# Kernel tuning notes

Measured on AMD Instinct MI355X. Metric: run time of the kernel, lower is better.

Reference implementation:

```python
import jax, jax.numpy as jnp
import numpy as np
import math

DIM, NH, HD = 4096, 32, 128
B, S = 2, 2048
MAX_SEQ, INIT_SLICE = 4096, 2048  # init_slice = max_seq_len - max_prompt_size
NEG = -1e9


def setup_inputs() -> dict:
    key = jax.random.key(0)
    ks = jax.random.split(key, 6)
    x = jax.random.normal(ks[0], (B, S, DIM), dtype=jnp.float32)
    scale = 1.0 / math.sqrt(DIM)
    wq = jax.random.normal(ks[1], (DIM, DIM), dtype=jnp.float32) * scale
    wk = jax.random.normal(ks[2], (DIM, DIM), dtype=jnp.float32) * scale
    wv = jax.random.normal(ks[3], (DIM, DIM), dtype=jnp.float32) * scale
    wo = jax.random.normal(ks[4], (DIM, DIM), dtype=jnp.float32) * scale
    # RoPE frequencies, viewed as real pairs [S, HD//2, 2] = (cos, sin)
    inv_freq = 1.0 / (10000.0 ** (jnp.arange(0, HD, 2, dtype=jnp.float32) / HD))
    ang = jnp.arange(S, dtype=jnp.float32)[:, None] * inv_freq[None, :]  # [S, HD//2]
    freqs_cis_real = jnp.stack([jnp.cos(ang), jnp.sin(ang)], axis=-1)
    # causal additive mask [1,1,S,S]
    mask = jnp.where(jnp.triu(jnp.ones((S, S), dtype=bool), k=1), NEG, 0.0)[None, None].astype(jnp.float32)
    cache_k = jnp.zeros((B, MAX_SEQ, NH, HD), dtype=jnp.float32)
    cache_v = jnp.zeros((B, MAX_SEQ, NH, HD), dtype=jnp.float32)
    return {"x": x, "freqs_cis_real": freqs_cis_real, "mask": mask,
            "wq": wq, "wk": wk, "wv": wv, "wo": wo,
            "cache_k": cache_k, "cache_v": cache_v, "slice_size": 2048}


def _apply_rotary(xq, xk, freqs_cis_real):
    # xq, xk: [b, s, h, d]; pairs along last dim are (real, imag)
    b, s, h, d = xq.shape
    fr = freqs_cis_real[None, :, None, :, 0]  # [1, s, 1, d//2]
    fi = freqs_cis_real[None, :, None, :, 1]

    def rot(t):
        t = t.reshape(b, s, h, d // 2, 2)
        tr, ti = t[..., 0], t[..., 1]
        out = jnp.stack([tr * fr - ti * fi, tr * fi + ti * fr], axis=-1)
        return out.reshape(b, s, h, d)

    return rot(xq), rot(xk)


def reference(x, freqs_cis_real, mask, wq, wk, wv, wo, cache_k, cache_v, slice_size):
    bsz, seqlen, _ = x.shape
    xq = (x @ wq.T).reshape(bsz, seqlen, NH, HD)
    xk = (x @ wk.T).reshape(bsz, seqlen, NH, HD)
    xv = (x @ wv.T).reshape(bsz, seqlen, NH, HD)
    xq, xk = _apply_rotary(xq, xk, freqs_cis_real)
    # prompt-phase (seqlen > 1) cache update: cat(cache[:, :init_slice], new)
    cache_k_new = jnp.concatenate([cache_k[:bsz, :INIT_SLICE], xk], axis=1)
    cache_v_new = jnp.concatenate([cache_v[:bsz, :INIT_SLICE], xv], axis=1)
    keys = cache_k_new[:, -slice_size:]    # [b, k, h, d]
    values = cache_v_new[:, -slice_size:]
    scores = jnp.einsum('bqhd,bkhd->bhqk', xq, keys) / math.sqrt(HD)
    scores = scores + mask
    probs = jax.nn.softmax(scores.astype(jnp.float32), axis=-1).astype(xq.dtype)
    out = jnp.einsum('bhqk,bkhd->bqhd', probs, values).reshape(bsz, seqlen, -1)
    return out @ wo.T
```

## Files before the change

### kernel.cpp

```cpp
#include <hip/hip_runtime.h>
#include <hip/hip_bf16.h>
#include <stdint.h>

#define SEQ   2048
#define NHEAD 32
#define HDIM  128
#define DMODEL 4096
#define MTOT  4096
#define RSCALE 0.08838834764831845f

typedef __hip_bfloat16 bf16_t;
typedef __attribute__((ext_vector_type(8))) short short8v;
typedef __attribute__((ext_vector_type(4))) short short4v;
typedef __attribute__((ext_vector_type(4))) float f32x4;
typedef __attribute__((ext_vector_type(2))) float f32x2;

typedef __attribute__((address_space(3))) void lds_void;
typedef __attribute__((address_space(1))) void gbl_void;
#define TO_LDS(p) ((lds_void*)(uint32_t)(uintptr_t)(p))
#define TO_GBL(p) ((gbl_void*)(uintptr_t)(p))
#define ASYNC_CP16(g, l) __builtin_amdgcn_global_load_lds(TO_GBL(g), TO_LDS(l), 16, 0, 0)

__device__ __forceinline__ float bf2f(short u) {
  union { uint32_t i; float f; } x; x.i = ((uint32_t)(uint16_t)u) << 16; return x.f;
}

__global__ __launch_bounds__(256) void cast4_f32_to_bf16(const float* __restrict__ s0,
                                                         const float* __restrict__ s1,
                                                         const float* __restrict__ s2,
                                                         const float* __restrict__ s3,
                                                         bf16_t* __restrict__ out) {
  const int w = blockIdx.y;
  const float* in = (w == 0) ? s0 : ((w == 1) ? s1 : ((w == 2) ? s2 : s3));
  bf16_t* o = out + (size_t)w * 16777216u;
  size_t i = (size_t)blockIdx.x * 256 + threadIdx.x;
  const f32x4* p = (const f32x4*)in + i * 2;
  f32x4 a = p[0], b = p[1];
  __align__(16) bf16_t tmp[8];
#pragma unroll
  for (int j = 0; j < 4; ++j) tmp[j]     = __float2bfloat16(a[j]);
#pragma unroll
  for (int j = 0; j < 4; ++j) tmp[4 + j] = __float2bfloat16(b[j]);
  *(short8v*)(o + i * 8) = *(const short8v*)tmp;
}

__global__ __launch_bounds__(256) void cast_f32_to_bf16(const float* __restrict__ in,
                                                        bf16_t* __restrict__ out) {
  size_t i = (size_t)blockIdx.x * 256 + threadIdx.x;
  const f32x4* p = (const f32x4*)in + i * 2;
  f32x4 a = p[0], b = p[1];
  __align__(16) bf16_t tmp[8];
#pragma unroll
  for (int j = 0; j < 4; ++j) tmp[j]     = __float2bfloat16(a[j]);
#pragma unroll
  for (int j = 0; j < 4; ++j) tmp[4 + j] = __float2bfloat16(b[j]);
  *(short8v*)(out + i * 8) = *(const short8v*)tmp;
}

#define VMW_(N) asm volatile("s_waitcnt vmcnt(" #N ")" ::: "memory")
#define VMW(N) VMW_(N)
#define SB0 __builtin_amdgcn_sched_barrier(0)

#define STAGE_A(mh_, X)                                                        \
  { const int tr_ = tid >> 3, c_ = tid & 7;                                    \
    _Pragma("unroll")                                                          \
    for (int i_ = 0; i_ < 2; ++i_) {                                           \
      const int row_ = (mh_) * 64 + i_ * 128 + tr_;                            \
      const int cg_ = c_ ^ (row_ & 7);                                         \
      ASYNC_CP16(gA0 + (size_t)row_ * 4096 + (size_t)(X) * 64 + cg_ * 8,       \
                 ldsc + (((X) & 1) << 16) + row_ * 128 + c_ * 16); } }

#define STAGE_B(nh_, X)                                                        \
  { const int tr_ = tid >> 3, c_ = tid & 7;                                    \
    _Pragma("unroll")                                                          \
    for (int i_ = 0; i_ < 2; ++i_) {                                           \
      const int row_ = i_ * 128 + (tr_ >> 5) * 64 + (nh_) * 32 + (tr_ & 31);   \
      const int cg_ = c_ ^ (row_ & 7);                                         \
      ASYNC_CP16(gB0 + (size_t)row_ * 4096 + (size_t)(X) * 64 + cg_ * 8,       \
                 ldsc + (((X) & 1) << 16) + 32768 + row_ * 128 + c_ * 16); } }

#define TILE4(T, DOSTG, VA, VB, VC)                                            \
  {                                                                            \
    const int sb = ((T) & 1) << 16;                                            \
    const int Xn = (T) + 1;                                                    \
    short8v a0[4][2], a1[4][2], b0[2][2], b1[2][2];                            \
                                                 \
    VMW(VA);                                                                   \
    __builtin_amdgcn_s_barrier();                                              \
    SB0;                                                                       \
    _Pragma("unroll") for (int m = 0; m < 4; ++m)                              \
      _Pragma("unroll") for (int kk = 0; kk < 2; ++kk)                         \
        a0[m][kk] = *(const short8v*)(ldsc + sb + aRow + m * 2048 + (kk ? cx1 : cx0)); \
    _Pragma("unroll") for (int n = 0; n < 2; ++n)                              \
      _Pragma("unroll") for (int kk = 0; kk < 2; ++kk)                         \
        b0[n][kk] = *(const short8v*)(ldsc + sb + bRow + n * 2048 + (kk ? cx1 : cx0)); \
    if (DOSTG) STAGE_A(0, Xn);                                                 \
    asm volatile("s_waitcnt lgkmcnt(0)" ::: "memory");                         \
    SB0;                                                                       \
    __builtin_amdgcn_s_setprio(1);                                             \
    _Pragma("unroll") for (int m = 0; m < 4; ++m)                              \
      _Pragma("unroll") for (int n = 0; n < 2; ++n)                            \
        _Pragma("unroll") for (int kk = 0; kk < 2; ++kk)                       \
          acc[m][n] = __builtin_amdgcn_mfma_f32_16x16x32_bf16(a0[m][kk], b0[n][kk], acc[m][n], 0, 0, 0); \
    __builtin_amdgcn_s_setprio(0);                                             \
                                                 \
    VMW(VB);                                                                   \
    __builtin_amdgcn_s_barrier();                                              \
    SB0;                                                                       \
    _Pragma("unroll") for (int n = 0; n < 2; ++n)                              \
      _Pragma("unroll") for (int kk = 0; kk < 2; ++kk)                         \
        b1[n][kk] = *(const short8v*)(ldsc + sb + bRow + 4096 + n * 2048 + (kk ? cx1 : cx0)); \
    if (DOSTG) STAGE_B(0, Xn);                                                 \
    asm volatile("s_waitcnt lgkmcnt(0)" ::: "memory");                         \
    SB0;                                                                       \
    __builtin_amdgcn_s_setprio(1);                                             \
    _Pragma("unroll") for (int m = 0; m < 4; ++m)                              \
      _Pragma("unroll") for (int n = 0; n < 2; ++n)                            \
        _Pragma("unroll") for (int kk = 0; kk < 2; ++kk)                       \
          acc[m][2 + n] = __builtin_amdgcn_mfma_f32_16x16x32_bf16(a0[m][kk], b1[n][kk], acc[m][2 + n], 0, 0, 0); \
    __builtin_amdgcn_s_setprio(0);                                             \
                                                 \
    VMW(VC);                                                                   \
    __builtin_amdgcn_s_barrier();                                              \
    SB0;                                                                       \
    _Pragma("unroll") for (int m = 0; m < 4; ++m)                              \
      _Pragma("unroll") for (int kk = 0; kk < 2; ++kk)                         \
        a1[m][kk] = *(const short8v*)(ldsc + sb + aRow + 8192 + m * 2048 + (kk ? cx1 : cx0)); \
    if (DOSTG) STAGE_B(1, Xn);                                                 \
    asm volatile("s_waitcnt lgkmcnt(0)" ::: "memory");                         \
    SB0;                                                                       \
    __builtin_amdgcn_s_setprio(1);                                             \
    _Pragma("unroll") for (int m = 0; m < 4; ++m)                              \
      _Pragma("unroll") for (int n = 0; n < 2; ++n)                            \
        _Pragma("unroll") for (int kk = 0; kk < 2; ++kk)                       \
          acc[4 + m][2 + n] = __builtin_amdgcn_mfma_f32_16x16x32_bf16(a1[m][kk], b1[n][kk], acc[4 + m][2 + n], 0, 0, 0); \
    __builtin_amdgcn_s_setprio(0);                                             \
                                     \
    if (DOSTG) STAGE_A(1, Xn);                                                 \
    __builtin_amdgcn_s_setprio(1);                                             \
    _Pragma("unroll") for (int m = 0; m < 4; ++m)                              \
      _Pragma("unroll") for (int n = 0; n < 2; ++n)                            \
        _Pragma("unroll") for (int kk = 0; kk < 2; ++kk)                       \
          acc[4 + m][n] = __builtin_amdgcn_mfma_f32_16x16x32_bf16(a1[m][kk], b0[n][kk], acc[4 + m][n], 0, 0, 0); \
    __builtin_amdgcn_s_setprio(0);                                             \
  }

template <int MODE>
__global__ __launch_bounds__(512, 2) void gemm_nt(const bf16_t* __restrict__ A,
                                                  const bf16_t* __restrict__ B0,
                                                  const bf16_t* __restrict__ B1,
                                                  const bf16_t* __restrict__ B2,
                                                  void* __restrict__ out0,
                                                  bf16_t* __restrict__ out1,
                                                  bf16_t* __restrict__ out2,
                                                  const float* __restrict__ freqs) {
  __shared__ __align__(16) char ldsbuf[131072];
  char* ldsc = ldsbuf;
  const int z = blockIdx.z;
  const bf16_t* __restrict__ Bm = (z == 0) ? B0 : (z == 1 ? B1 : B2);
  const int tid = threadIdx.x;
  const int wave = tid >> 6, lane = tid & 63;
  const int bid = blockIdx.x;
  const int xcd = bid & 7, idx = bid >> 3;
  const int bm = xcd * 2 + (idx >> 4);
  const int bn = idx & 15;
  const int wr = wave >> 2, wc = wave & 3;
  const int r = lane & 15, g = lane >> 4;

  f32x4 acc[8][4] = {};

  const bf16_t* gA0 = A  + (size_t)bm * 256 * 4096;
  const bf16_t* gB0 = Bm + (size_t)bn * 256 * 4096;

  const int swz = r & 7;
  const int cx0 = (g ^ swz) << 4;
  const int cx1 = ((4 + g) ^ swz) << 4;
  const int aRow = (wr * 128 + r) * 128;
  const int bRow = 32768 + (wc * 64 + r) * 128;

  STAGE_A(0, 0);
  STAGE_B(0, 0);
  STAGE_B(1, 0);
  STAGE_A(1, 0);

  for (int T = 0; T < 63; ++T) TILE4(T, 1, 4, 4, 4);
  TILE4(63, 0, 4, 2, 0);

  const int row0 = bm * 256 + wr * 128 + g * 4;
  const int col0 = bn * 256 + wc * 64;

  if (MODE == 0) {
    float* C = (float*)out0;
#pragma unroll
    for (int m = 0; m < 8; ++m)
#pragma unroll
      for (int n = 0; n < 4; ++n)
#pragma unroll
        for (int j = 0; j < 4; ++j)
          C[(size_t)(row0 + m * 16 + j) * 4096 + col0 + n * 16 + r] = acc[m][n][j];
  } else if (z == 2) {
    bf16_t* VT = out2;
#pragma unroll
    for (int m = 0; m < 8; ++m) {
      const int row = row0 + m * 16;
      const int b = row >> 11, s = row & 2047;
#pragma unroll
      for (int n = 0; n < 4; ++n) {
        const int col = col0 + n * 16 + r;
        const int h = col >> 7, d = col & 127;
        __align__(8) bf16_t tp[4];
#pragma unroll
        for (int j = 0; j < 4; ++j) tp[j] = __float2bfloat16(acc[m][n][j]);
        *(short4v*)&VT[((size_t)(b * 32 + h) * 128 + d) * 2048 + s] = *(const short4v*)tp;
      }
    }
  } else if (z == 0) {
    bf16_t* dst = (bf16_t*)out0;
#pragma unroll
    for (int m = 0; m < 8; ++m)
#pragma unroll
      for (int j = 0; j < 4; ++j) {
        const int row = row0 + m * 16 + j;
        const int b = row >> 11, s = row & 2047;
#pragma unroll
        for (int n = 0; n < 4; ++n) {
          const int col = col0 + n * 16 + r;
          const int h = col >> 7, d = col & 127;
          dst[((size_t)(b * 32 + h) * 2048 + s) * 128 + d] = __float2bfloat16(acc[m][n][j]);
        }
      }
  } else {
    bf16_t* dst = out1;
    const float sgn = (r & 1) ? 1.0f : -1.0f;
#pragma unroll
    for (int m = 0; m < 8; ++m)
#pragma unroll
      for (int j = 0; j < 4; ++j) {
        const int row = row0 + m * 16 + j;
        const int b = row >> 11, s = row & 2047;
#pragma unroll
        for (int n = 0; n < 4; ++n) {
          const int col = col0 + n * 16 + r;
          const int h = col >> 7, d = col & 127;
          const float self = acc[m][n][j];
          const float part = __shfl_xor(self, 1, 64);
          const float* fp = freqs + (size_t)s * 128 + (d >> 1) * 2;
          const float frv = fp[0];
          const float fiv = fp[1] * sgn;
          dst[((size_t)(b * 32 + h) * 2048 + s) * 128 + d] =
              __float2bfloat16(self * frv + part * fiv);
        }
      }
  }
}

__global__ __launch_bounds__(512) void attn_kernel(const bf16_t* __restrict__ qrot,
                                                   const bf16_t* __restrict__ krot,
                                                   const bf16_t* __restrict__ vt,
                                                   const float* __restrict__ freqs,
                                                   bf16_t* __restrict__ att) {
  __shared__ bf16_t Kls[2][64 * 128];
  __shared__ bf16_t Vls[2][128 * 64];
  __shared__ bf16_t Pls[8][16 * 64];

  const int lid  = blockIdx.x;
  const int xcd  = lid & 7;
  const int kk_  = lid >> 3;
  const int bh   = xcd + 8 * ((kk_ >> 4) & 7);
  const int qidx = 15 - (kk_ & 15);
  const int warp = threadIdx.x >> 6;
  const int lane = threadIdx.x & 63;
  const int r = lane & 15, g = lane >> 4;

  const bf16_t* __restrict__ Q  = qrot + (size_t)bh * 2048 * 128;
  const bf16_t* __restrict__ Kp = krot + (size_t)bh * 2048 * 128;
  const bf16_t* __restrict__ Vt = vt   + (size_t)bh * 128 * 2048;
  char* __restrict__ Pb = (char*)&Pls[warp][0];

  const int qB = qidx * 128 + warp * 16;
  const int ntiles = 2 * qidx + 2;
  const int psw = (r & 7) << 4;

  short8v qf[4];
  {
    const int s = qB + r;
    const float* fbase = freqs + (size_t)s * 128;
#pragma unroll
    for (int kk = 0; kk < 4; ++kk) {
      short8v qraw = *(const short8v*)&Q[(size_t)s * 128 + kk * 32 + g * 8];
      __align__(16) bf16_t qt[8];
#pragma unroll
      for (int i = 0; i < 4; ++i) {
        const int p = kk * 16 + g * 4 + i;
        f32x2 cs = *(const f32x2*)(fbase + p * 2);
        const float a = bf2f(qraw[2 * i]), b = bf2f(qraw[2 * i + 1]);
        qt[2 * i]     = __float2bfloat16((a * cs[0] - b * cs[1]) * RSCALE);
        qt[2 * i + 1] = __float2bfloat16((a * cs[1] + b * cs[0]) * RSCALE);
      }
      qf[kk] = *(const short8v*)qt;
    }
  }

  float l = 0.f;
  f32x4 o[8];
#pragma unroll
  for (int n2 = 0; n2 < 8; ++n2) o[n2] = f32x4{0.f, 0.f, 0.f, 0.f};

  const int rA = lane >> 4, cA = lane & 15;
  const int rB = lane >> 3, cB = lane & 7;
  const int swz = (r & 7) << 4;

  auto STG = [&](int kb_, int buf) {
#pragma unroll
    for (int i = 0; i < 2; ++i) {
      const int krow = warp * 8 + i * 4 + rA;
      const int kcol = 8 * (cA ^ (krow & 7));
      ASYNC_CP16(Kp + (size_t)(kb_ + krow) * 128 + kcol,
                 (char*)&Kls[buf][0] + (size_t)(krow * 128 + cA * 8) * 2);
    }
#pragma unroll
    for (int i = 0; i < 2; ++i) {
      const int vrow = warp * 16 + i * 8 + rB;
      const int vcol = 8 * (cB ^ rB);
      ASYNC_CP16(Vt + (size_t)vrow * 2048 + kb_ + vcol,
                 (char*)&Vls[buf][0] + (size_t)(vrow * 64 + cB * 8) * 2);
    }
  };

  STG(0, 0);
  VMW(0);
  __builtin_amdgcn_s_barrier();
  int cur = 0;
  for (int t = 0; t < ntiles; ++t) {
    const int kb = t * 64;
    if (t + 1 < ntiles) STG(kb + 64, cur ^ 1);

    if (kb <= qB + 15) {
      const char* Kc = (const char*)&Kls[cur][0];
      const char* Vc = (const char*)&Vls[cur][0];
      f32x4 sacc[4];
#pragma unroll
      for (int n = 0; n < 4; ++n) sacc[n] = f32x4{0.f, 0.f, 0.f, 0.f};
#pragma unroll
      for (int n = 0; n < 4; ++n)
#pragma unroll
        for (int kk = 0; kk < 4; ++kk) {
          short8v kf = *(const short8v*)(Kc + (n * 16 + r) * 256 + ((kk * 64 + g * 16) ^ swz));
          sacc[n] = __builtin_amdgcn_mfma_f32_16x16x32_bf16(kf, qf[kk], sacc[n], 0, 0, 0);
        }

      float p[16];
#pragma unroll
      for (int n = 0; n < 4; ++n)
#pragma unroll
        for (int j = 0; j < 4; ++j)
          p[n * 4 + j] = __expf(sacc[n][j]);

      if (kb + 63 > qB) {
        const int qa = qB + r;
#pragma unroll
        for (int n = 0; n < 4; ++n)
#pragma unroll
          for (int j = 0; j < 4; ++j)
            if (kb + n * 16 + g * 4 + j > qa) p[n * 4 + j] = 0.f;
      }

      {
        float ts[8];
#pragma unroll
        for (int i = 0; i < 8; ++i) ts[i] = p[i] + p[i + 8];
#pragma unroll
        for (int i = 0; i < 4; ++i) ts[i] += ts[i + 4];
        float rs = (ts[0] + ts[1]) + (ts[2] + ts[3]);
        rs += __shfl_xor(rs, 16, 64);
        rs += __shfl_xor(rs, 32, 64);
        l += rs;
      }

#pragma unroll
      for (int n = 0; n < 4; ++n) {
        __align__(8) bf16_t tp[4];
#pragma unroll
        for (int j = 0; j < 4; ++j) tp[j] = __float2bfloat16(p[n * 4 + j]);
        *(short4v*)(Pb + r * 128 + ((n * 32 + g * 8) ^ psw)) = *(const short4v*)tp;
      }

#pragma unroll
      for (int kk2 = 0; kk2 < 2; ++kk2) {
        short8v pf = *(const short8v*)(Pb + r * 128 + ((kk2 * 64 + g * 16) ^ psw));
#pragma unroll
        for (int n2 = 0; n2 < 8; ++n2) {
          short8v vf = *(const short8v*)(Vc + (n2 * 16 + r) * 128 + ((kk2 * 64 + g * 16) ^ swz));
          o[n2] = __builtin_amdgcn_mfma_f32_16x16x32_bf16(pf, vf, o[n2], 0, 0, 0);
        }
      }
    }

    if (t + 1 < ntiles) {
      VMW(0);
      __builtin_amdgcn_s_barrier();
    }
    cur ^= 1;
  }

  float lq[4];
#pragma unroll
  for (int j = 0; j < 4; ++j) lq[j] = 1.0f / __shfl(l, g * 4 + j, 64);
  const int b = bh >> 5, h = bh & 31;
#pragma unroll
  for (int n2 = 0; n2 < 8; ++n2)
#pragma unroll
    for (int j = 0; j < 4; ++j)
      att[((size_t)(b * 2048 + qB + g * 4 + j)) * 4096 + h * 128 + n2 * 16 + r] =
          __float2bfloat16(o[n2][j] * lq[j]);
}

extern "C" void kernel_launch(void* const* d_in, const int* in_sizes, int n_in,
                              void* d_out, int out_size, void* d_ws, size_t ws_size,
                              hipStream_t stream) {
  (void)in_sizes; (void)n_in; (void)out_size; (void)ws_size;
  const float* x  = (const float*)d_in[0];
  const float* fr = (const float*)d_in[1];
  const float* wq = (const float*)d_in[3];
  const float* wk = (const float*)d_in[4];
  const float* wv = (const float*)d_in[5];
  const float* wo = (const float*)d_in[6];

  char* ws = (char*)d_ws;
  const size_t MB32 = 33554432;
  bf16_t* xb   = (bf16_t*)(ws + 0 * MB32);
  bf16_t* wqb  = (bf16_t*)(ws + 1 * MB32);
  bf16_t* wkb  = (bf16_t*)(ws + 2 * MB32);
  bf16_t* wvb  = (bf16_t*)(ws + 3 * MB32);
  bf16_t* qrot = (bf16_t*)(ws + 4 * MB32);
  bf16_t* krot = (bf16_t*)(ws + 5 * MB32);
  bf16_t* vtp  = (bf16_t*)(ws + 6 * MB32);

  cast4_f32_to_bf16<<<dim3(8192, 4), 256, 0, stream>>>(x, wq, wk, wv, xb);

  gemm_nt<1><<<dim3(256, 1, 3), 512, 0, stream>>>(xb, wqb, wkb, wvb,
                                                  (void*)qrot, krot, vtp, fr);

  bf16_t* wob  = wqb;
  bf16_t* attb = xb;
  cast_f32_to_bf16<<<8192, 256, 0, stream>>>(wo, wob);

  attn_kernel<<<1024, 512, 0, stream>>>(qrot, krot, vtp, fr, attb);

  gemm_nt<0><<<dim3(256, 1, 1), 512, 0, stream>>>(attb, wob, wob, wob,
                                                  d_out, nullptr, nullptr, nullptr);
}
```

Measured before the change: 647.0 us.

## Fold wo cast into attention launch and restructure GEMM tile barriers

The separate wo fp32-to-bf16 cast kernel is removed. Its work now runs in 512 extra blocks appended to the attention launch, which saves one launch and lets the cast overlap with attention. The GEMM inner tile drops one of its three barrier phases by loading the b1 and a1 fragments earlier, with adjusted vmcnt waits. The block-to-tile mapping is also changed to group 4x8 tiles per XCD for better L2 locality. The risks are more register pressure from the early fragment loads and a possible LDS hazard from the looser waits.

```diff
diff --git a/kernel.cpp b/kernel.cpp
--- a/kernel.cpp
+++ b/kernel.cpp
@@ -44,19 +44,6 @@
   *(short8v*)(o + i * 8) = *(const short8v*)tmp;
 }
 
-__global__ __launch_bounds__(256) void cast_f32_to_bf16(const float* __restrict__ in,
-                                                        bf16_t* __restrict__ out) {
-  size_t i = (size_t)blockIdx.x * 256 + threadIdx.x;
-  const f32x4* p = (const f32x4*)in + i * 2;
-  f32x4 a = p[0], b = p[1];
-  __align__(16) bf16_t tmp[8];
-#pragma unroll
-  for (int j = 0; j < 4; ++j) tmp[j]     = __float2bfloat16(a[j]);
-#pragma unroll
-  for (int j = 0; j < 4; ++j) tmp[4 + j] = __float2bfloat16(b[j]);
-  *(short8v*)(out + i * 8) = *(const short8v*)tmp;
-}
-
 #define VMW_(N) asm volatile("s_waitcnt vmcnt(" #N ")" ::: "memory")
 #define VMW(N) VMW_(N)
 #define SB0 __builtin_amdgcn_sched_barrier(0)
@@ -79,13 +66,13 @@
       ASYNC_CP16(gB0 + (size_t)row_ * 4096 + (size_t)(X) * 64 + cg_ * 8,       \
                  ldsc + (((X) & 1) << 16) + 32768 + row_ * 128 + c_ * 16); } }
 
-#define TILE4(T, DOSTG, VA, VB, VC)                                            \
+#define TILE4(T, DOSTG, V1, V2)                                                \
   {                                                                            \
     const int sb = ((T) & 1) << 16;                                            \
     const int Xn = (T) + 1;                                                    \
     short8v a0[4][2], a1[4][2], b0[2][2], b1[2][2];                            \
-                                                 \
-    VMW(VA);                                                                   \
+                                   \
+    VMW(V1);                                                                   \
     __builtin_amdgcn_s_barrier();                                              \
     SB0;                                                                       \
     _Pragma("unroll") for (int m = 0; m < 4; ++m)                              \
@@ -94,6 +81,9 @@
     _Pragma("unroll") for (int n = 0; n < 2; ++n)                              \
       _Pragma("unroll") for (int kk = 0; kk < 2; ++kk)                         \
         b0[n][kk] = *(const short8v*)(ldsc + sb + bRow + n * 2048 + (kk ? cx1 : cx0)); \
+    _Pragma("unroll") for (int n = 0; n < 2; ++n)                              \
+      _Pragma("unroll") for (int kk = 0; kk < 2; ++kk)                         \
+        b1[n][kk] = *(const short8v*)(ldsc + sb + bRow + 4096 + n * 2048 + (kk ? cx1 : cx0)); \
     if (DOSTG) STAGE_A(0, Xn);                                                 \
     asm volatile("s_waitcnt lgkmcnt(0)" ::: "memory");                         \
     SB0;                                                                       \
@@ -103,15 +93,14 @@
         _Pragma("unroll") for (int kk = 0; kk < 2; ++kk)                       \
           acc[m][n] = __builtin_amdgcn_mfma_f32_16x16x32_bf16(a0[m][kk], b0[n][kk], acc[m][n], 0, 0, 0); \
     __builtin_amdgcn_s_setprio(0);                                             \
-                                                 \
-    VMW(VB);                                                                   \
+      \
+    VMW(V2);                                                                   \
     __builtin_amdgcn_s_barrier();                                              \
     SB0;                                                                       \
-    _Pragma("unroll") for (int n = 0; n < 2; ++n)                              \
+    _Pragma("unroll") for (int m = 0; m < 4; ++m)                              \
       _Pragma("unroll") for (int kk = 0; kk < 2; ++kk)                         \
-        b1[n][kk] = *(const short8v*)(ldsc + sb + bRow + 4096 + n * 2048 + (kk ? cx1 : cx0)); \
+        a1[m][kk] = *(const short8v*)(ldsc + sb + aRow + 8192 + m * 2048 + (kk ? cx1 : cx0)); \
     if (DOSTG) STAGE_B(0, Xn);                                                 \
-    asm volatile("s_waitcnt lgkmcnt(0)" ::: "memory");                         \
     SB0;                                                                       \
     __builtin_amdgcn_s_setprio(1);                                             \
     _Pragma("unroll") for (int m = 0; m < 4; ++m)                              \
@@ -119,13 +108,7 @@
         _Pragma("unroll") for (int kk = 0; kk < 2; ++kk)                       \
           acc[m][2 + n] = __builtin_amdgcn_mfma_f32_16x16x32_bf16(a0[m][kk], b1[n][kk], acc[m][2 + n], 0, 0, 0); \
     __builtin_amdgcn_s_setprio(0);                                             \
-                                                 \
-    VMW(VC);                                                                   \
-    __builtin_amdgcn_s_barrier();                                              \
-    SB0;                                                                       \
-    _Pragma("unroll") for (int m = 0; m < 4; ++m)                              \
-      _Pragma("unroll") for (int kk = 0; kk < 2; ++kk)                         \
-        a1[m][kk] = *(const short8v*)(ldsc + sb + aRow + 8192 + m * 2048 + (kk ? cx1 : cx0)); \
+                                 \
     if (DOSTG) STAGE_B(1, Xn);                                                 \
     asm volatile("s_waitcnt lgkmcnt(0)" ::: "memory");                         \
     SB0;                                                                       \
@@ -135,7 +118,7 @@
         _Pragma("unroll") for (int kk = 0; kk < 2; ++kk)                       \
           acc[4 + m][2 + n] = __builtin_amdgcn_mfma_f32_16x16x32_bf16(a1[m][kk], b1[n][kk], acc[4 + m][2 + n], 0, 0, 0); \
     __builtin_amdgcn_s_setprio(0);                                             \
-                                     \
+                                                 \
     if (DOSTG) STAGE_A(1, Xn);                                                 \
     __builtin_amdgcn_s_setprio(1);                                             \
     _Pragma("unroll") for (int m = 0; m < 4; ++m)                              \
@@ -162,8 +145,8 @@
   const int wave = tid >> 6, lane = tid & 63;
   const int bid = blockIdx.x;
   const int xcd = bid & 7, idx = bid >> 3;
-  const int bm = xcd * 2 + (idx >> 4);
-  const int bn = idx & 15;
+  const int bm = (xcd >> 1) * 4 + (idx >> 3);
+  const int bn = (xcd & 1) * 8 + (idx & 7);
   const int wr = wave >> 2, wc = wave & 3;
   const int r = lane & 15, g = lane >> 4;
 
@@ -183,8 +166,8 @@
   STAGE_B(1, 0);
   STAGE_A(1, 0);
 
-  for (int T = 0; T < 63; ++T) TILE4(T, 1, 4, 4, 4);
-  TILE4(63, 0, 4, 2, 0);
+  for (int T = 0; T < 63; ++T) TILE4(T, 1, 2, 2);
+  TILE4(63, 0, 2, 0);
 
   const int row0 = bm * 256 + wr * 128 + g * 4;
   const int col0 = bn * 256 + wc * 64;
@@ -258,10 +241,30 @@
                                                    const bf16_t* __restrict__ krot,
                                                    const bf16_t* __restrict__ vt,
                                                    const float* __restrict__ freqs,
-                                                   bf16_t* __restrict__ att) {
+                                                   bf16_t* __restrict__ att,
+                                                   const float* __restrict__ wo_src,
+                                                   bf16_t* __restrict__ wo_dst) {
   __shared__ bf16_t Kls[2][64 * 128];
   __shared__ bf16_t Vls[2][128 * 64];
   __shared__ bf16_t Pls[8][16 * 64];
+
+  if (blockIdx.x >= 1024) {
+    const int cb = blockIdx.x - 1024;
+    const int tid = threadIdx.x;
+#pragma unroll
+    for (int p = 0; p < 8; ++p) {
+      size_t i = ((size_t)p * 512 + cb) * 512 + tid;
+      const f32x4* pp = (const f32x4*)wo_src + i * 2;
+      f32x4 a = pp[0], b = pp[1];
+      __align__(16) bf16_t tmp[8];
+#pragma unroll
+      for (int j = 0; j < 4; ++j) tmp[j]     = __float2bfloat16(a[j]);
+#pragma unroll
+      for (int j = 0; j < 4; ++j) tmp[4 + j] = __float2bfloat16(b[j]);
+      *(short8v*)(wo_dst + i * 8) = *(const short8v*)tmp;
+    }
+    return;
+  }
 
   const int lid  = blockIdx.x;
   const int xcd  = lid & 7;
@@ -443,9 +446,8 @@
 
   bf16_t* wob  = wqb;
   bf16_t* attb = xb;
-  cast_f32_to_bf16<<<8192, 256, 0, stream>>>(wo, wob);
-
-  attn_kernel<<<1024, 512, 0, stream>>>(qrot, krot, vtp, fr, attb);
+
+  attn_kernel<<<1536, 512, 0, stream>>>(qrot, krot, vtp, fr, attb, wo, wob);
 
   gemm_nt<0><<<dim3(256, 1, 1), 512, 0, stream>>>(attb, wob, wob, wob,
                                                   d_out, nullptr, nullptr, nullptr);
```

New measurement: 635.0 us. Within noise of the previous version (-1.9%).
